# Performance work log

Hardware: AMD Instinct MI355X
Metric: run time of the kernel (lower is better)

The kernel has to match this reference:

```python
import jax, jax.numpy as jnp
import numpy as np


def setup_inputs() -> dict:
    key = jax.random.key(0)
    B, C, L = 32, 512, 4096
    inputs = jax.random.normal(key, (B, C, L), dtype=jnp.float32)
    return {"inputs": inputs, "top_k": 8}


def reference(inputs, top_k):
    # inputs: [B, C, L]. Select top_k values along last dim, keep original order.
    _, top_idxs = jax.lax.top_k(inputs, top_k)          # [B, C, k] indices of k largest
    sorted_idxs = jnp.sort(top_idxs, axis=2)            # restore positional order
    return jnp.take_along_axis(inputs, sorted_idxs, axis=2)  # [B, C, k]
```

## Files before the change

kernel.cpp:

```cpp
#include <hip/hip_runtime.h>
#include <cstdint>

#define ROW_LEN 4096
#define KSEL 8
#define NT 256
#define EPT 16

#define CEDA(a, i, j) { float x_ = a[i], y_ = a[j]; a[i] = fmaxf(x_, y_); a[j] = fminf(x_, y_); }

#define SORT8D(a, o) \
    CEDA(a,o+0,o+1) CEDA(a,o+2,o+3) CEDA(a,o+4,o+5) CEDA(a,o+6,o+7) \
    CEDA(a,o+0,o+2) CEDA(a,o+1,o+3) CEDA(a,o+4,o+6) CEDA(a,o+5,o+7) \
    CEDA(a,o+1,o+2) CEDA(a,o+5,o+6) \
    CEDA(a,o+0,o+4) CEDA(a,o+1,o+5) CEDA(a,o+2,o+6) CEDA(a,o+3,o+7) \
    CEDA(a,o+2,o+4) CEDA(a,o+3,o+5) \
    CEDA(a,o+1,o+2) CEDA(a,o+3,o+4) CEDA(a,o+5,o+6)

#define BMERGE8D(a) \
    CEDA(a,0,4) CEDA(a,1,5) CEDA(a,2,6) CEDA(a,3,7) \
    CEDA(a,0,2) CEDA(a,1,3) CEDA(a,4,6) CEDA(a,5,7) \
    CEDA(a,0,1) CEDA(a,2,3) CEDA(a,4,5) CEDA(a,6,7)

__global__ __launch_bounds__(NT) void kmax_kernel(const float* __restrict__ in,
                                                  float* __restrict__ out) {
    const int row  = blockIdx.x;
    const int tid  = threadIdx.x;
    const int lane = tid & 63;
    const int wave = tid >> 6;

    const float4* p4 = reinterpret_cast<const float4*>(in + (size_t)row * ROW_LEN + (size_t)tid * EPT);

    float k[EPT];
#pragma unroll
    for (int j = 0; j < 4; ++j) {
        float4 a = p4[j];
        k[j * 4 + 0] = a.x;
        k[j * 4 + 1] = a.y;
        k[j * 4 + 2] = a.z;
        k[j * 4 + 3] = a.w;
    }

    float t[EPT];
#pragma unroll
    for (int s = 0; s < EPT; ++s) t[s] = k[s];
    SORT8D(t, 0)
    SORT8D(t, 8)
#pragma unroll
    for (int s = 0; s < 8; ++s) t[s] = fmaxf(t[s], t[15 - s]);
    BMERGE8D(t)

#pragma unroll
    for (int off = 1; off < 64; off <<= 1) {
        float o[8];
#pragma unroll
        for (int s = 0; s < 8; ++s) o[s] = __shfl_xor(t[s], off, 64);
#pragma unroll
        for (int s = 0; s < 8; ++s) t[s] = fmaxf(t[s], o[7 - s]);
        BMERGE8D(t)
    }

    __shared__ float    W[4][KSEL];
    __shared__ unsigned swsum[4];

    if (lane == 0) {
        float4* wp = reinterpret_cast<float4*>(&W[wave][0]);
        wp[0] = make_float4(t[0], t[1], t[2], t[3]);
        wp[1] = make_float4(t[4], t[5], t[6], t[7]);
    }
    __syncthreads();

    float A[8], B[8];
#pragma unroll
    for (int s = 0; s < 8; ++s) A[s] = fmaxf(W[0][s], W[1][7 - s]);
    BMERGE8D(A)
#pragma unroll
    for (int s = 0; s < 8; ++s) B[s] = fmaxf(W[2][s], W[3][7 - s]);
    BMERGE8D(B)
    float T = fmaxf(A[0], B[7]);
#pragma unroll
    for (int s = 1; s < 8; ++s) T = fminf(T, fmaxf(A[s], B[7 - s]));

    int cgt = 0, ceq = 0;
#pragma unroll
    for (int s = 0; s < EPT; ++s) {
        cgt += (k[s] > T);
        ceq += (k[s] == T);
    }
    unsigned packed = ((unsigned)cgt << 16) | (unsigned)ceq;
    unsigned p = packed;
#pragma unroll
    for (int off = 1; off < 64; off <<= 1) {
        unsigned o = (unsigned)__shfl_up((int)p, off, 64);
        if (lane >= off) p += o;
    }
    if (lane == 63) swsum[wave] = p;
    __syncthreads();
    unsigned basep = 0, total = 0;
#pragma unroll
    for (int w = 0; w < 4; ++w) {
        unsigned ws = swsum[w];
        total += ws;
        if (w < wave) basep += ws;
    }
    unsigned excl  = basep + p - packed;
    int totgt = (int)(total >> 16), toteq = (int)(total & 0xFFFFu);
    int pgt   = (int)(excl  >> 16), peq   = (int)(excl  & 0xFFFFu);
    int Q      = KSEL - totgt;
    int mybase = pgt + (peq < Q ? peq : Q);
    float* op  = out + (size_t)row * KSEL + mybase;

    if (totgt + toteq == KSEL) {
#pragma unroll
        for (int s = 0; s < EPT; ++s) {
            if (k[s] >= T) { *op++ = k[s]; }
        }
    } else {
        int myq = Q - peq; myq = myq < 0 ? 0 : myq;
        int eqSeen = 0;
#pragma unroll
        for (int s = 0; s < EPT; ++s) {
            bool iseq = (k[s] == T);
            bool sel  = (k[s] > T) || (iseq && (eqSeen < myq));
            eqSeen += iseq;
            if (sel) { *op++ = k[s]; }
        }
    }
}

extern "C" void kernel_launch(void* const* d_in, const int* in_sizes, int n_in,
                              void* d_out, int out_size, void* d_ws, size_t ws_size,
                              hipStream_t stream) {
    const float* in  = (const float*)d_in[0];
    float*       out = (float*)d_out;
    const int rows = in_sizes[0] / ROW_LEN;
    kmax_kernel<<<rows, NT, 0, stream>>>(in, out);
}
```

Measured before the change: 361.2 us.

## Replace bitonic top-k merge with candidate filtering and radix-select threshold

Drops the per-thread sorting networks and the shuffle-based bitonic merges. Values above a fixed cutoff (2.30) are collected into a small shared candidate buffer with atomics, and one wave runs a 32-bit radix select by ballot on those candidates to find the k-th largest threshold. If the candidate count is below k or overflows the buffer, a slower exact block-wide radix select over all elements is used instead. The prefix-sum shuffle scan is also replaced with per-bit ballot/popcount counting. The fast path depends on the input distribution, here normally distributed values, putting only a few dozen elements above the cutoff per row; other inputs fall back to a path with 64 block barriers.

```diff
diff --git a/kernel.cpp b/kernel.cpp
--- a/kernel.cpp
+++ b/kernel.cpp
@@ -5,21 +5,17 @@
 #define KSEL 8
 #define NT 256
 #define EPT 16
+#define C0 2.30f
+#define CANDCAP 128
 
-#define CEDA(a, i, j) { float x_ = a[i], y_ = a[j]; a[i] = fmaxf(x_, y_); a[j] = fminf(x_, y_); }
-
-#define SORT8D(a, o) \
-    CEDA(a,o+0,o+1) CEDA(a,o+2,o+3) CEDA(a,o+4,o+5) CEDA(a,o+6,o+7) \
-    CEDA(a,o+0,o+2) CEDA(a,o+1,o+3) CEDA(a,o+4,o+6) CEDA(a,o+5,o+7) \
-    CEDA(a,o+1,o+2) CEDA(a,o+5,o+6) \
-    CEDA(a,o+0,o+4) CEDA(a,o+1,o+5) CEDA(a,o+2,o+6) CEDA(a,o+3,o+7) \
-    CEDA(a,o+2,o+4) CEDA(a,o+3,o+5) \
-    CEDA(a,o+1,o+2) CEDA(a,o+3,o+4) CEDA(a,o+5,o+6)
-
-#define BMERGE8D(a) \
-    CEDA(a,0,4) CEDA(a,1,5) CEDA(a,2,6) CEDA(a,3,7) \
-    CEDA(a,0,2) CEDA(a,1,3) CEDA(a,4,6) CEDA(a,5,7) \
-    CEDA(a,0,1) CEDA(a,2,3) CEDA(a,4,5) CEDA(a,6,7)
+__device__ inline unsigned ordkey(float f) {
+    int t = __float_as_int(f);
+    return (unsigned)(t ^ ((t >> 31) | 0x80000000));
+}
+__device__ inline float unkey(unsigned u) {
+    int t = (int)u;
+    return __int_as_float(t < 0 ? (t ^ 0x80000000) : ~t);
+}
 
 __global__ __launch_bounds__(NT) void kmax_kernel(const float* __restrict__ in,
                                                   float* __restrict__ out) {
@@ -28,8 +24,13 @@
     const int lane = tid & 63;
     const int wave = tid >> 6;
 
+    __shared__ float    cand[CANDCAP];
+    __shared__ int      scnt;
+    __shared__ unsigned swsum[4];
+
+    if (tid == 0) scnt = 0;
+
     const float4* p4 = reinterpret_cast<const float4*>(in + (size_t)row * ROW_LEN + (size_t)tid * EPT);
-
     float k[EPT];
 #pragma unroll
     for (int j = 0; j < 4; ++j) {
@@ -39,46 +40,51 @@
         k[j * 4 + 2] = a.z;
         k[j * 4 + 3] = a.w;
     }
-
-    float t[EPT];
-#pragma unroll
-    for (int s = 0; s < EPT; ++s) t[s] = k[s];
-    SORT8D(t, 0)
-    SORT8D(t, 8)
-#pragma unroll
-    for (int s = 0; s < 8; ++s) t[s] = fmaxf(t[s], t[15 - s]);
-    BMERGE8D(t)
+    __syncthreads();
 
 #pragma unroll
-    for (int off = 1; off < 64; off <<= 1) {
-        float o[8];
-#pragma unroll
-        for (int s = 0; s < 8; ++s) o[s] = __shfl_xor(t[s], off, 64);
-#pragma unroll
-        for (int s = 0; s < 8; ++s) t[s] = fmaxf(t[s], o[7 - s]);
-        BMERGE8D(t)
-    }
-
-    __shared__ float    W[4][KSEL];
-    __shared__ unsigned swsum[4];
-
-    if (lane == 0) {
-        float4* wp = reinterpret_cast<float4*>(&W[wave][0]);
-        wp[0] = make_float4(t[0], t[1], t[2], t[3]);
-        wp[1] = make_float4(t[4], t[5], t[6], t[7]);
+    for (int s = 0; s < EPT; ++s) {
+        if (k[s] > C0) {
+            int pos = atomicAdd(&scnt, 1);
+            if (pos < CANDCAP) cand[pos] = k[s];
+        }
     }
     __syncthreads();
 
-    float A[8], B[8];
+    const int cnt = scnt;
+    unsigned Tkey;
+    if (cnt >= KSEL && cnt <= CANDCAP) {
+        float f0 = cand[lane];
+        float f1 = cand[lane + 64];
+        unsigned c0 = (lane      < cnt) ? ordkey(f0) : 0u;
+        unsigned c1 = (lane + 64 < cnt) ? ordkey(f1) : 0u;
+        unsigned T = 0;
 #pragma unroll
-    for (int s = 0; s < 8; ++s) A[s] = fmaxf(W[0][s], W[1][7 - s]);
-    BMERGE8D(A)
+        for (int b = 31; b >= 0; --b) {
+            unsigned c = T | (1u << b);
+            int n = __popcll(__ballot(c0 >= c)) + __popcll(__ballot(c1 >= c));
+            if (n >= KSEL) T = c;
+        }
+        Tkey = T;
+    } else {
+        unsigned kk[EPT];
 #pragma unroll
-    for (int s = 0; s < 8; ++s) B[s] = fmaxf(W[2][s], W[3][7 - s]);
-    BMERGE8D(B)
-    float T = fmaxf(A[0], B[7]);
+        for (int s = 0; s < EPT; ++s) kk[s] = ordkey(k[s]);
+        unsigned T = 0;
+        for (int b = 31; b >= 0; --b) {
+            unsigned c = T | (1u << b);
+            int n = 0;
 #pragma unroll
-    for (int s = 1; s < 8; ++s) T = fminf(T, fmaxf(A[s], B[7 - s]));
+            for (int s = 0; s < EPT; ++s) n += __popcll(__ballot(kk[s] >= c));
+            if (lane == 0) swsum[wave] = (unsigned)n;
+            __syncthreads();
+            n = (int)(swsum[0] + swsum[1] + swsum[2] + swsum[3]);
+            __syncthreads();
+            if (n >= KSEL) T = c;
+        }
+        Tkey = T;
+    }
+    const float T = unkey(Tkey);
 
     int cgt = 0, ceq = 0;
 #pragma unroll
@@ -86,28 +92,36 @@
         cgt += (k[s] > T);
         ceq += (k[s] == T);
     }
-    unsigned packed = ((unsigned)cgt << 16) | (unsigned)ceq;
-    unsigned p = packed;
+    const unsigned long long lt = (1ull << lane) - 1ull;
+    int exGt = 0, totGt = 0;
 #pragma unroll
-    for (int off = 1; off < 64; off <<= 1) {
-        unsigned o = (unsigned)__shfl_up((int)p, off, 64);
-        if (lane >= off) p += o;
+    for (int b = 0; b < 3; ++b) {
+        unsigned long long m = __ballot((cgt >> b) & 1);
+        exGt  += __popcll(m & lt) << b;
+        totGt += __popcll(m) << b;
     }
-    if (lane == 63) swsum[wave] = p;
+    int exEq = 0, totEq = 0;
+#pragma unroll
+    for (int b = 0; b < 5; ++b) {
+        unsigned long long m = __ballot((ceq >> b) & 1);
+        exEq  += __popcll(m & lt) << b;
+        totEq += __popcll(m) << b;
+    }
+    if (lane == 0) swsum[wave] = ((unsigned)totGt << 16) | (unsigned)totEq;
     __syncthreads();
-    unsigned basep = 0, total = 0;
+    unsigned base = 0, tot = 0;
 #pragma unroll
     for (int w = 0; w < 4; ++w) {
-        unsigned ws = swsum[w];
-        total += ws;
-        if (w < wave) basep += ws;
+        unsigned v = swsum[w];
+        tot += v;
+        if (w < wave) base += v;
     }
-    unsigned excl  = basep + p - packed;
-    int totgt = (int)(total >> 16), toteq = (int)(total & 0xFFFFu);
-    int pgt   = (int)(excl  >> 16), peq   = (int)(excl  & 0xFFFFu);
-    int Q      = KSEL - totgt;
-    int mybase = pgt + (peq < Q ? peq : Q);
-    float* op  = out + (size_t)row * KSEL + mybase;
+    const int totgt = (int)(tot >> 16), toteq = (int)(tot & 0xFFFFu);
+    const int pgt = (int)(base >> 16) + exGt;
+    const int peq = (int)(base & 0xFFFFu) + exEq;
+    const int Q = KSEL - totgt;
+    const int mybase = pgt + (peq < Q ? peq : Q);
+    float* op = out + (size_t)row * KSEL + mybase;
 
     if (totgt + toteq == KSEL) {
 #pragma unroll
```

New measurement: 354.2 us. No clear change (-1.9%).
